# Kernel optimization log

Hardware: AMD Instinct MI355X
Metric: run time of the kernel (lower is better)

Reference implementation:

```python
import jax, jax.numpy as jnp
import numpy as np

B = 1024
NIF = 2048   # n_image_features
V = 10000    # vocab_size
E = 512      # embedding_dim
H = 1024     # hidden_size
L = 32       # max_sentence_length
ND = 3       # num distractors


def _lstm_cell(x, h, c, Wih, Whh, bih, bhh):
    # torch LSTMCell: gates ordered i, f, g, o
    g = x @ Wih.T + bih + h @ Whh.T + bhh
    i, f, gc, o = jnp.split(g, 4, axis=-1)
    c = jax.nn.sigmoid(f) * c + jax.nn.sigmoid(i) * jnp.tanh(gc)
    h = jax.nn.sigmoid(o) * jnp.tanh(c)
    return h, c


def setup_inputs() -> dict:
    key = jax.random.key(0)
    ks = jax.random.split(key, 20)
    s = 0.02
    inp = {
        "target": jax.random.normal(ks[0], (B, NIF), jnp.float32),
        "distractors": jax.random.normal(ks[1], (ND, B, NIF), jnp.float32),
        "start_token_idx": 1,
        "max_sentence_length": L,
        # Sender params
        "W_aff": s * jax.random.normal(ks[2], (H, NIF), jnp.float32),
        "b_aff": jnp.zeros((H,), jnp.float32),
        "emb_s": s * jax.random.normal(ks[3], (V, E), jnp.float32),
        "Wih_s": s * jax.random.normal(ks[4], (4 * H, E), jnp.float32),
        "Whh_s": s * jax.random.normal(ks[5], (4 * H, H), jnp.float32),
        "bih_s": jnp.zeros((4 * H,), jnp.float32),
        "bhh_s": jnp.zeros((4 * H,), jnp.float32),
        "Wp": s * jax.random.normal(ks[6], (V, H), jnp.float32),
        "bp": jnp.zeros((V,), jnp.float32),
        # Receiver params
        "emb_r": s * jax.random.normal(ks[7], (V, E), jnp.float32),
        "Wih_r": s * jax.random.normal(ks[8], (4 * H, E), jnp.float32),
        "Whh_r": s * jax.random.normal(ks[9], (4 * H, H), jnp.float32),
        "bih_r": jnp.zeros((4 * H,), jnp.float32),
        "bhh_r": jnp.zeros((4 * H,), jnp.float32),
        "W_out": s * jax.random.normal(ks[10], (NIF, H), jnp.float32),
        "b_out": jnp.zeros((NIF,), jnp.float32),
    }
    return inp


def reference(target, distractors, start_token_idx, max_sentence_length,
              W_aff, b_aff, emb_s, Wih_s, Whh_s, bih_s, bhh_s, Wp, bp,
              emb_r, Wih_r, Whh_r, bih_r, bhh_r, W_out, b_out):
    Bt = target.shape[0]

    # ---- Sender: greedy decode (eval-mode argmax, matching greedy=True) ----
    h0 = target @ W_aff.T + b_aff
    c0 = jnp.zeros_like(h0)
    w0 = emb_s[jnp.full((Bt,), start_token_idx, dtype=jnp.int32)]

    def send_step(carry, _):
        h, c, w = carry
        h, c = _lstm_cell(w, h, c, Wih_s, Whh_s, bih_s, bhh_s)
        logits = h @ Wp.T + bp                         # [B, V]
        idx = jnp.argmax(logits, axis=-1)              # greedy token
        logp = jnp.take_along_axis(jax.nn.log_softmax(logits, axis=-1),
                                   idx[:, None], axis=-1)[:, 0]
        w = emb_s[idx]
        return (h, c, w), (idx, logp)

    _, (message, logps) = jax.lax.scan(send_step, (h0, c0, w0), None,
                                       length=max_sentence_length)
    message = message.T            # [B, L]
    log_prob = logps[-1]           # log_prob of last sampled word, [B]

    # ---- Receiver: encode message ----
    hr = jnp.zeros((Bt, H), jnp.float32)
    cr = jnp.zeros((Bt, H), jnp.float32)

    def recv_step(carry, w_idx):
        h, c = carry
        h, c = _lstm_cell(emb_r[w_idx], h, c, Wih_r, Whh_r, bih_r, bhh_r)
        return (h, c), None

    (hr, cr), _ = jax.lax.scan(recv_step, (hr, cr), message.T)
    r = hr @ W_out.T + b_out       # [B, NIF]

    # ---- Hinge loss over distractors ----
    r_T = r.T                                       # [NIF, B]
    t_r = target @ r_T                              # [B, B]
    d_r = jnp.einsum('nbf,fc->nbc', distractors, r_T)  # [ND, B, B]
    loss = jnp.sum(jnp.maximum(0.0, 1.0 - t_r[None] + d_r), axis=0)  # [B, B]
    loss = -loss * log_prob        # broadcast [B] over last dim, as in torch
    return jnp.mean(loss)
```

## Files before the change

kernel.cpp:

```cpp
#include <hip/hip_runtime.h>
#include <hip/hip_bf16.h>
#include <cstdint>
#include <cstddef>

#define Bc   1024
#define NIFc 2048
#define Vc   10000
#define Ec   512
#define Hc   1024
#define Lc   32
#define NDc  3
#define G4c  4096
#define NTv  79
#define TMLD 80
#define XLD  3584
#define XOFF 512
#define RLD  1536

typedef __attribute__((ext_vector_type(4))) float f32x4;
typedef __attribute__((ext_vector_type(8))) short s16x8;
typedef __attribute__((ext_vector_type(4))) short s16x4;

__device__ __host__ __forceinline__ int rperm_orig(int p) {
    return ((p >> 4) & 3) * Hc + (p >> 6) * 16 + (p & 15);
}

#define GBM 128
#define GBN 128
#define GBK 64

struct __align__(16) GemmSmem {
    __hip_bfloat16 As[GBM * GBK];
    __hip_bfloat16 Ws[GBN * GBK];
    float smax[GBM];
};

__device__ __forceinline__ void gld_lds16(void* lds, const void* g) {
    __builtin_amdgcn_global_load_lds(
        (const __attribute__((address_space(1))) unsigned int*)g,
        (__attribute__((address_space(3))) unsigned int*)lds,
        16, 0, 0);
}

template<int OBF>
__device__ __forceinline__ void gemm_body(
    GemmSmem& sm,
    const __hip_bfloat16* __restrict__ A, int lda,
    const __hip_bfloat16* __restrict__ W, int ldw,
    const float* __restrict__ bias, void* __restrict__ Cv,
    int M, int N, int K, int bx, int by,
    float* __restrict__ tile_max, int tmld)
{
    __hip_bfloat16* As = sm.As;
    __hip_bfloat16* Ws = sm.Ws;
    float* smax = sm.smax;

    const int tid  = threadIdx.x;
    const int lane = tid & 63;
    const int wave = tid >> 6;
    const int m0 = by * GBM;
    const int n0 = bx * GBN;

    const __hip_bfloat16* ag[4];
    const __hip_bfloat16* wg[4];
    #pragma unroll
    for (int r = 0; r < 4; ++r) {
        int p = r * 256 + tid;
        int m = p >> 3;
        int q = (p & 7) ^ (m & 7);
        int am = m0 + m; if (am >= M) am = M - 1;
        ag[r] = A + (size_t)am * lda + q * 8;
        int wn = n0 + m; if (wn >= N) wn = N - 1;
        wg[r] = W + (size_t)wn * ldw + q * 8;
    }

    f32x4 acc[4][4];
    #pragma unroll
    for (int i = 0; i < 4; ++i)
        #pragma unroll
        for (int j = 0; j < 4; ++j)
            acc[i][j] = (f32x4)(0.0f);

    const int hm = (wave & 1) << 6;
    const int hn = (wave >> 1) << 6;
    const int lm = lane & 15;
    const int quad = lane >> 4;

    const int nk = K >> 6;
    for (int kt = 0; kt < nk; ++kt) {
        __syncthreads();
        #pragma unroll
        for (int r = 0; r < 4; ++r) {
            int ldsbase = (r * 256 + wave * 64) * 8;
            gld_lds16(As + ldsbase, ag[r]);
            gld_lds16(Ws + ldsbase, wg[r]);
            ag[r] += GBK;
            wg[r] += GBK;
        }
        __syncthreads();
        #pragma unroll
        for (int c = 0; c < 2; ++c) {
            s16x8 af[4], wf[4];
            int q = c * 4 + quad;
            #pragma unroll
            for (int i = 0; i < 4; ++i) {
                int m = hm + i * 16 + lm;
                af[i] = *(const s16x8*)(As + ((m << 3) + (q ^ (m & 7))) * 8);
                int n = hn + i * 16 + lm;
                wf[i] = *(const s16x8*)(Ws + ((n << 3) + (q ^ (n & 7))) * 8);
            }
            #pragma unroll
            for (int i = 0; i < 4; ++i)
                #pragma unroll
                for (int j = 0; j < 4; ++j)
                    acc[i][j] = __builtin_amdgcn_mfma_f32_16x16x32_bf16(
                        af[i], wf[j], acc[i][j], 0, 0, 0);
        }
    }

    float rowmax[4][4];
    #pragma unroll
    for (int i = 0; i < 4; ++i)
        #pragma unroll
        for (int rr = 0; rr < 4; ++rr)
            rowmax[i][rr] = -__builtin_inff();

    #pragma unroll
    for (int i = 0; i < 4; ++i) {
        int mbase = m0 + hm + i * 16 + quad * 4;
        #pragma unroll
        for (int j = 0; j < 4; ++j) {
            int n = n0 + hn + j * 16 + lm;
            if (n < N) {
                float bv = bias ? bias[n] : 0.0f;
                #pragma unroll
                for (int rr = 0; rr < 4; ++rr) {
                    float v = acc[i][j][rr] + bv;
                    float vs = v;
                    if (OBF) {
                        __hip_bfloat16 vb = __float2bfloat16(v);
                        vs = __bfloat162float(vb);
                        if (mbase + rr < M)
                            ((__hip_bfloat16*)Cv)[(size_t)(mbase + rr) * N + n] = vb;
                    } else {
                        if (mbase + rr < M)
                            ((float*)Cv)[(size_t)(mbase + rr) * N + n] = v;
                    }
                    rowmax[i][rr] = fmaxf(rowmax[i][rr], vs);
                }
            }
        }
    }

    if (tile_max) {
        #pragma unroll
        for (int i = 0; i < 4; ++i)
            #pragma unroll
            for (int rr = 0; rr < 4; ++rr) {
                float v = rowmax[i][rr];
                v = fmaxf(v, __shfl_xor(v, 1));
                v = fmaxf(v, __shfl_xor(v, 2));
                v = fmaxf(v, __shfl_xor(v, 4));
                v = fmaxf(v, __shfl_xor(v, 8));
                rowmax[i][rr] = v;
            }
        __syncthreads();
        if (hn == 0 && lm == 0) {
            #pragma unroll
            for (int i = 0; i < 4; ++i)
                #pragma unroll
                for (int rr = 0; rr < 4; ++rr)
                    smax[hm + i * 16 + quad * 4 + rr] = rowmax[i][rr];
        }
        __syncthreads();
        if (hn == 64 && lm == 0) {
            #pragma unroll
            for (int i = 0; i < 4; ++i)
                #pragma unroll
                for (int rr = 0; rr < 4; ++rr) {
                    int r = hm + i * 16 + quad * 4 + rr;
                    smax[r] = fmaxf(smax[r], rowmax[i][rr]);
                }
        }
        __syncthreads();
        if (tid < GBM)
            tile_max[(size_t)(m0 + tid) * tmld + bx] = smax[tid];
    }
}

__device__ __forceinline__ void recv_gemm_cell_body(
    GemmSmem& sm,
    const __hip_bfloat16* __restrict__ A,
    const __hip_bfloat16* __restrict__ W,
    const float* __restrict__ biasp,
    const __hip_bfloat16* __restrict__ Xg,
    const int* __restrict__ tok,
    float* __restrict__ cr,
    __hip_bfloat16* __restrict__ xh_out,
    int bx, int by)
{
    __hip_bfloat16* As = sm.As;
    __hip_bfloat16* Ws = sm.Ws;

    const int tid  = threadIdx.x;
    const int lane = tid & 63;
    const int wave = tid >> 6;
    const int m0 = by * GBM;
    const int n0 = bx * GBN;

    const __hip_bfloat16* ag[4];
    const __hip_bfloat16* wg[4];
    #pragma unroll
    for (int r = 0; r < 4; ++r) {
        int p = r * 256 + tid;
        int m = p >> 3;
        int q = (p & 7) ^ (m & 7);
        ag[r] = A + (size_t)(m0 + m) * RLD + q * 8;
        wg[r] = W + (size_t)(n0 + m) * RLD + q * 8;
    }

    f32x4 acc[4][4];
    #pragma unroll
    for (int i = 0; i < 4; ++i)
        #pragma unroll
        for (int j = 0; j < 4; ++j)
            acc[i][j] = (f32x4)(0.0f);

    const int hm = (wave & 1) << 6;
    const int hn = (wave >> 1) << 6;
    const int lm = lane & 15;
    const int quad = lane >> 4;

    for (int kt = 0; kt < Hc / GBK; ++kt) {
        __syncthreads();
        #pragma unroll
        for (int r = 0; r < 4; ++r) {
            int ldsbase = (r * 256 + wave * 64) * 8;
            gld_lds16(As + ldsbase, ag[r]);
            gld_lds16(Ws + ldsbase, wg[r]);
            ag[r] += GBK;
            wg[r] += GBK;
        }
        __syncthreads();
        #pragma unroll
        for (int c = 0; c < 2; ++c) {
            s16x8 af[4], wf[4];
            int q = c * 4 + quad;
            #pragma unroll
            for (int i = 0; i < 4; ++i) {
                int m = hm + i * 16 + lm;
                af[i] = *(const s16x8*)(As + ((m << 3) + (q ^ (m & 7))) * 8);
                int n = hn + i * 16 + lm;
                wf[i] = *(const s16x8*)(Ws + ((n << 3) + (q ^ (n & 7))) * 8);
            }
            #pragma unroll
            for (int i = 0; i < 4; ++i)
                #pragma unroll
                for (int j = 0; j < 4; ++j)
                    acc[i][j] = __builtin_amdgcn_mfma_f32_16x16x32_bf16(
                        af[i], wf[j], acc[i][j], 0, 0, 0);
        }
    }

    const int u = ((n0 + hn) >> 6) * 16 + lm;
    int pc[4];
    float bv[4];
    #pragma unroll
    for (int g = 0; g < 4; ++g) {
        pc[g] = n0 + hn + g * 16 + lm;
        bv[g] = biasp[pc[g]];
    }
    #pragma unroll
    for (int i = 0; i < 4; ++i) {
        #pragma unroll
        for (int rr = 0; rr < 4; ++rr) {
            int b = m0 + hm + i * 16 + quad * 4 + rr;
            const __hip_bfloat16* xr = Xg + (size_t)tok[b] * G4c;
            float gi = acc[i][0][rr] + bv[0] + __bfloat162float(xr[pc[0]]);
            float gf = acc[i][1][rr] + bv[1] + __bfloat162float(xr[pc[1]]);
            float gg = acc[i][2][rr] + bv[2] + __bfloat162float(xr[pc[2]]);
            float go = acc[i][3][rr] + bv[3] + __bfloat162float(xr[pc[3]]);
            float si = 1.0f / (1.0f + expf(-gi));
            float sf = 1.0f / (1.0f + expf(-gf));
            float so = 1.0f / (1.0f + expf(-go));
            size_t cix = (size_t)b * Hc + u;
            float cc = sf * cr[cix] + si * tanhf(gg);
            cr[cix] = cc;
            xh_out[(size_t)b * RLD + Ec + u] = __float2bfloat16(so * tanhf(cc));
        }
    }
}

__global__ __launch_bounds__(256) void gemm_recv_final(
    const __hip_bfloat16* __restrict__ A, const __hip_bfloat16* __restrict__ W,
    const float* __restrict__ biasp, const __hip_bfloat16* __restrict__ Xg,
    const int* __restrict__ tok, float* __restrict__ cr,
    __hip_bfloat16* __restrict__ xh_out)
{
    __shared__ GemmSmem sm;
    recv_gemm_cell_body(sm, A, W, biasp, Xg, tok, cr, xh_out,
                        blockIdx.x & 31, blockIdx.x >> 5);
}

__global__ __launch_bounds__(256) void gemm_bf16_tn(
    const __hip_bfloat16* __restrict__ A, int lda,
    const __hip_bfloat16* __restrict__ W, int ldw,
    const float* __restrict__ bias, float* __restrict__ C,
    int M, int N, int K, float* __restrict__ tile_max, int tmld)
{
    __shared__ GemmSmem sm;
    gemm_body<0>(sm, A, lda, W, ldw, bias, C, M, N, K, blockIdx.x, blockIdx.y,
                 tile_max, tmld);
}

__global__ __launch_bounds__(256) void gemm_bf16_sk2(
    const __hip_bfloat16* __restrict__ A, int lda,
    const __hip_bfloat16* __restrict__ W, int ldw,
    float* __restrict__ Cpart, int M, int N, int Ksub)
{
    __shared__ GemmSmem sm;
    int z = blockIdx.z;
    gemm_body<0>(sm, A + (size_t)z * Ksub, lda, W + (size_t)z * Ksub, ldw,
                 nullptr, Cpart + (size_t)z * M * N, M, N, Ksub, blockIdx.x,
                 blockIdx.y, nullptr, 0);
}

__global__ __launch_bounds__(256) void gemm_tab_h0(
    int nbS, int nbR,
    const __hip_bfloat16* __restrict__ embS, const __hip_bfloat16* __restrict__ embR,
    const __hip_bfloat16* __restrict__ W3x, const __hip_bfloat16* __restrict__ Wr,
    __hip_bfloat16* __restrict__ XgS, __hip_bfloat16* __restrict__ XgR,
    const __hip_bfloat16* __restrict__ target3,
    const __hip_bfloat16* __restrict__ W_aff3, float* __restrict__ gates_p)
{
    __shared__ GemmSmem sm;
    int bid = blockIdx.x;
    if (bid < nbS) {
        gemm_body<1>(sm, embS, Ec, W3x, XLD, nullptr, XgS,
                     Vc, G4c, Ec, bid & 31, bid >> 5, nullptr, 0);
    } else if (bid < nbS + nbR) {
        int rem = bid - nbS;
        gemm_body<1>(sm, embR, Ec, Wr, RLD, nullptr, XgR,
                     Vc, G4c, Ec, rem & 31, rem >> 5, nullptr, 0);
    } else {
        int r2 = bid - nbS - nbR;
        int z = r2 >> 6, rem = r2 & 63;
        gemm_body<0>(sm, target3 + (size_t)z * 3072, 6144,
                     W_aff3 + (size_t)z * 3072, 6144, nullptr,
                     gates_p + (size_t)z * Bc * Hc,
                     Bc, Hc, 3072, rem & 7, rem >> 3, nullptr, 0);
    }
}

template<int LOGBF>
__global__ __launch_bounds__(256) void gemm_fused_step(
    int nb_g,
    const __hip_bfloat16* __restrict__ Ag, const __hip_bfloat16* __restrict__ Wg,
    float* __restrict__ Cg,
    const __hip_bfloat16* __restrict__ Al, const __hip_bfloat16* __restrict__ Wl,
    const float* __restrict__ bl, void* __restrict__ Cl,
    float* __restrict__ tmax)
{
    __shared__ GemmSmem sm;
    int bid = blockIdx.x;
    if (bid < nb_g) {
        gemm_body<0>(sm, Ag, XLD, Wg, XLD, nullptr, Cg,
                     Bc, G4c, 3072, bid & 31, bid >> 5, nullptr, 0);
    } else {
        int rem = bid - nb_g;
        int by = rem / NTv, bx = rem - by * NTv;
        gemm_body<LOGBF>(sm, Al, XLD, Wl, Hc, bl, Cl, Bc, Vc, Hc, bx, by,
                         tmax, TMLD);
    }
}

#define PC0  2097152
#define PC1  6291456
#define PC2  16531456
#define PC3  18628608
#define PC4  20725760
#define PC5  22822912
#define PC6  27017216
#define PC7  29114368
#define PC8  29118464
#define PC9  29122560
#define PC10 34242560
#define PC11 39362560
#define PC12 41459712
#define PC13 47751168

__global__ __launch_bounds__(256) void prep_all_kernel(
    const float* __restrict__ Wih_s, const float* __restrict__ Whh_s,
    const float* __restrict__ Wp, const float* __restrict__ target,
    const float* __restrict__ W_aff, const float* __restrict__ Wih_r,
    const float* __restrict__ Whh_r, const float* __restrict__ W_out,
    const float* __restrict__ bih_s, const float* __restrict__ bhh_s,
    const float* __restrict__ bih_r, const float* __restrict__ bhh_r,
    const float* __restrict__ emb_s, const float* __restrict__ emb_r,
    const float* __restrict__ distr,
    __hip_bfloat16* __restrict__ W3x, __hip_bfloat16* __restrict__ Wp_b,
    __hip_bfloat16* __restrict__ target3, __hip_bfloat16* __restrict__ W_aff3,
    __hip_bfloat16* __restrict__ WihWhh_r, __hip_bfloat16* __restrict__ W_out_b,
    float* __restrict__ bias_s, float* __restrict__ bias_r,
    __hip_bfloat16* __restrict__ embS, __hip_bfloat16* __restrict__ embR,
    __hip_bfloat16* __restrict__ A4b)
{
    int i = blockIdx.x * 256 + threadIdx.x;
    if (i < PC0) {
        W3x[(size_t)(i / Ec) * XLD + (i % Ec)] = __float2bfloat16(Wih_s[i]);
    } else if (i < PC1) {
        int k = i - PC0; int m = k / Hc, c = k - m * Hc;
        float v = Whh_s[k];
        __hip_bfloat16 hi = __float2bfloat16(v);
        float lo = v - __bfloat162float(hi);
        __hip_bfloat16* row = W3x + (size_t)m * XLD + XOFF;
        row[c] = hi; row[Hc + c] = hi; row[2 * Hc + c] = __float2bfloat16(lo);
    } else if (i < PC2) {
        int k = i - PC1;
        Wp_b[k] = __float2bfloat16(Wp[k]);
    } else if (i < PC3) {
        int k = i - PC2; int m = k / NIFc, c = k - m * NIFc;
        float v = target[k];
        __hip_bfloat16 hi = __float2bfloat16(v);
        float lo = v - __bfloat162float(hi);
        __hip_bfloat16* row = target3 + (size_t)m * 6144;
        row[c] = hi; row[NIFc + c] = __float2bfloat16(lo); row[2 * NIFc + c] = hi;
    } else if (i < PC4) {
        int k = i - PC3; int m = k / NIFc, c = k - m * NIFc;
        float v = W_aff[k];
        __hip_bfloat16 hi = __float2bfloat16(v);
        float lo = v - __bfloat162float(hi);
        __hip_bfloat16* row = W_aff3 + (size_t)m * 6144;
        row[c] = hi; row[NIFc + c] = hi; row[2 * NIFc + c] = __float2bfloat16(lo);
    } else if (i < PC5) {
        int k = i - PC4; int p = k / Ec, c = k - p * Ec;
        WihWhh_r[(size_t)p * RLD + c] =
            __float2bfloat16(Wih_r[(size_t)rperm_orig(p) * Ec + c]);
    } else if (i < PC6) {
        int k = i - PC5; int p = k / Hc, c = k - p * Hc;
        WihWhh_r[(size_t)p * RLD + Ec + c] =
            __float2bfloat16(Whh_r[(size_t)rperm_orig(p) * Hc + c]);
    } else if (i < PC7) {
        int k = i - PC6;
        W_out_b[k] = __float2bfloat16(W_out[k]);
    } else if (i < PC8) {
        int k = i - PC7;
        bias_s[k] = bih_s[k] + bhh_s[k];
    } else if (i < PC9) {
        int k = i - PC8; int s = rperm_orig(k);
        bias_r[k] = bih_r[s] + bhh_r[s];
    } else if (i < PC10) {
        int k = i - PC9;
        embS[k] = __float2bfloat16(emb_s[k]);
    } else if (i < PC11) {
        int k = i - PC10;
        embR[k] = __float2bfloat16(emb_r[k]);
    } else if (i < PC12) {
        int k = i - PC11;
        A4b[k] = __float2bfloat16(target[k]);
    } else if (i < PC13) {
        int k = i - PC12;
        A4b[(size_t)Bc * NIFc + k] = __float2bfloat16(distr[k]);
    }
}

__global__ __launch_bounds__(256) void cast2d_kernel(
    const float* __restrict__ in, int ldin,
    __hip_bfloat16* __restrict__ out, int ldo, int coff, int M, int K)
{
    int i = blockIdx.x * 256 + threadIdx.x;
    if (i >= M * K) return;
    int m = i / K, k = i - m * K;
    out[(size_t)m * ldo + coff + k] = __float2bfloat16(in[(size_t)m * ldin + k]);
}

__global__ __launch_bounds__(256) void gather_cast_kernel(
    const float* __restrict__ emb, int E, const int* __restrict__ idx,
    int stride, __hip_bfloat16* __restrict__ out, int ldo, int coff, int Brows)
{
    int i = blockIdx.x * 256 + threadIdx.x;
    if (i >= Brows * E) return;
    int b = i / E, k = i - b * E;
    out[(size_t)b * ldo + coff + k] =
        __float2bfloat16(emb[(size_t)idx[(size_t)b * stride] * E + k]);
}

__device__ __forceinline__ short bf16bits(float x) {
    __hip_bfloat16 t = __float2bfloat16(x);
    return *reinterpret_cast<short*>(&t);
}

__device__ __forceinline__ float b16f(short s) {
    return __bfloat162float(*reinterpret_cast<__hip_bfloat16*>(&s));
}

__global__ __launch_bounds__(256) void lstm_fused_s(
    const float* __restrict__ gp0, const float* __restrict__ gp1,
    const float* __restrict__ bias, float* __restrict__ h,
    float* __restrict__ c, __hip_bfloat16* __restrict__ h3x,
    const __hip_bfloat16* __restrict__ xg, const int* __restrict__ tok,
    int tstride)
{
    int i = blockIdx.x * 256 + threadIdx.x;
    if (i >= Bc * Hc / 4) return;
    int b = i >> 8;
    int j = (i & 255) * 4;
    size_t g0 = (size_t)b * G4c + j;
    f32x4 gi = *(const f32x4*)(gp0 + g0) + *(const f32x4*)(gp1 + g0)
             + *(const f32x4*)(bias + j);
    f32x4 gf = *(const f32x4*)(gp0 + g0 + Hc) + *(const f32x4*)(gp1 + g0 + Hc)
             + *(const f32x4*)(bias + Hc + j);
    f32x4 gg = *(const f32x4*)(gp0 + g0 + 2 * Hc) + *(const f32x4*)(gp1 + g0 + 2 * Hc)
             + *(const f32x4*)(bias + 2 * Hc + j);
    f32x4 go = *(const f32x4*)(gp0 + g0 + 3 * Hc) + *(const f32x4*)(gp1 + g0 + 3 * Hc)
             + *(const f32x4*)(bias + 3 * Hc + j);
    if (xg) {
        const __hip_bfloat16* xr = xg + (size_t)tok[(size_t)b * tstride] * G4c;
        s16x4 xi = *(const s16x4*)(xr + j);
        s16x4 xf = *(const s16x4*)(xr + Hc + j);
        s16x4 xc = *(const s16x4*)(xr + 2 * Hc + j);
        s16x4 xo = *(const s16x4*)(xr + 3 * Hc + j);
        #pragma unroll
        for (int k = 0; k < 4; ++k) {
            gi[k] += b16f(xi[k]);
            gf[k] += b16f(xf[k]);
            gg[k] += b16f(xc[k]);
            go[k] += b16f(xo[k]);
        }
    }
    size_t hix = (size_t)b * Hc + j;
    f32x4 cv = *(const f32x4*)(c + hix);
    f32x4 cn, hv;
    s16x4 hi4, lo4;
    #pragma unroll
    for (int k = 0; k < 4; ++k) {
        float si = 1.0f / (1.0f + expf(-gi[k]));
        float sf = 1.0f / (1.0f + expf(-gf[k]));
        float so = 1.0f / (1.0f + expf(-go[k]));
        float cc = sf * cv[k] + si * tanhf(gg[k]);
        cn[k] = cc;
        float hh = so * tanhf(cc);
        hv[k] = hh;
        hi4[k] = bf16bits(hh);
        lo4[k] = bf16bits(hh - __bfloat162float(__float2bfloat16(hh)));
    }
    *(f32x4*)(c + hix) = cn;
    *(f32x4*)(h + hix) = hv;
    __hip_bfloat16* row = h3x + (size_t)b * XLD + XOFF;
    *(s16x4*)(row + j) = hi4;
    *(s16x4*)(row + Hc + j) = lo4;
    *(s16x4*)(row + 2 * Hc + j) = hi4;
}

__global__ __launch_bounds__(256) void combine_h0_kernel(
    const float* __restrict__ p0, const float* __restrict__ p1,
    const float* __restrict__ bias, float* __restrict__ h,
    __hip_bfloat16* __restrict__ h3x)
{
    int i = blockIdx.x * 256 + threadIdx.x;
    if (i >= Bc * Hc / 4) return;
    int b = i >> 8;
    int j = (i & 255) * 4;
    size_t ix = (size_t)b * Hc + j;
    f32x4 v = *(const f32x4*)(p0 + ix) + *(const f32x4*)(p1 + ix)
            + *(const f32x4*)(bias + j);
    *(f32x4*)(h + ix) = v;
    s16x4 hi4, lo4;
    #pragma unroll
    for (int k = 0; k < 4; ++k) {
        hi4[k] = bf16bits(v[k]);
        lo4[k] = bf16bits(v[k] - __bfloat162float(__float2bfloat16(v[k])));
    }
    __hip_bfloat16* row = h3x + (size_t)b * XLD + XOFF;
    *(s16x4*)(row + j) = hi4;
    *(s16x4*)(row + Hc + j) = lo4;
    *(s16x4*)(row + 2 * Hc + j) = hi4;
}

__global__ __launch_bounds__(256) void lstm_fused_r(
    const float* __restrict__ gp0, const float* __restrict__ gp1,
    const float* __restrict__ bias, float* __restrict__ h,
    float* __restrict__ c, __hip_bfloat16* __restrict__ xh_r,
    const __hip_bfloat16* __restrict__ xg, const int* __restrict__ tok,
    int has_g, const float* __restrict__ emb, const int* __restrict__ msg_next)
{
    int i = blockIdx.x * 256 + threadIdx.x;
    if (i >= Bc * Hc / 4) return;
    int b = i >> 8;
    int j = (i & 255) * 4;
    int pb = (j >> 4) * 64 + (j & 15);
    f32x4 gi = *(const f32x4*)(bias + pb);
    f32x4 gf = *(const f32x4*)(bias + pb + 16);
    f32x4 gg = *(const f32x4*)(bias + pb + 32);
    f32x4 go = *(const f32x4*)(bias + pb + 48);
    if (has_g) {
        size_t g0 = (size_t)b * G4c + pb;
        gi += *(const f32x4*)(gp0 + g0) + *(const f32x4*)(gp1 + g0);
        gf += *(const f32x4*)(gp0 + g0 + 16) + *(const f32x4*)(gp1 + g0 + 16);
        gg += *(const f32x4*)(gp0 + g0 + 32) + *(const f32x4*)(gp1 + g0 + 32);
        go += *(const f32x4*)(gp0 + g0 + 48) + *(const f32x4*)(gp1 + g0 + 48);
    }
    if (xg) {
        const __hip_bfloat16* xr = xg + (size_t)tok[b] * G4c;
        s16x4 xi = *(const s16x4*)(xr + pb);
        s16x4 xf = *(const s16x4*)(xr + pb + 16);
        s16x4 xc = *(const s16x4*)(xr + pb + 32);
        s16x4 xo = *(const s16x4*)(xr + pb + 48);
        #pragma unroll
        for (int k = 0; k < 4; ++k) {
            gi[k] += b16f(xi[k]);
            gf[k] += b16f(xf[k]);
            gg[k] += b16f(xc[k]);
            go[k] += b16f(xo[k]);
        }
    }
    size_t hix = (size_t)b * Hc + j;
    f32x4 cv = *(const f32x4*)(c + hix);
    f32x4 cn, hv;
    s16x4 hb4;
    #pragma unroll
    for (int k = 0; k < 4; ++k) {
        float si = 1.0f / (1.0f + expf(-gi[k]));
        float sf = 1.0f / (1.0f + expf(-gf[k]));
        float so = 1.0f / (1.0f + expf(-go[k]));
        float cc = sf * cv[k] + si * tanhf(gg[k]);
        cn[k] = cc;
        float hh = so * tanhf(cc);
        hv[k] = hh;
        hb4[k] = bf16bits(hh);
    }
    *(f32x4*)(c + hix) = cn;
    *(f32x4*)(h + hix) = hv;
    *(s16x4*)(xh_r + (size_t)b * RLD + Ec + j) = hb4;
    if (!xg && msg_next && j < Ec) {
        int t2 = msg_next[b];
        f32x4 e = *(const f32x4*)(emb + (size_t)t2 * Ec + j);
        s16x4 eb;
        #pragma unroll
        for (int k = 0; k < 4; ++k) eb[k] = bf16bits(e[k]);
        *(s16x4*)(xh_r + (size_t)b * RLD + j) = eb;
    }
}

__global__ __launch_bounds__(256) void argmax_rescore_v3(
    const float* __restrict__ logits, const float* __restrict__ tmax,
    const float* __restrict__ h, const float* __restrict__ Wp,
    const float* __restrict__ bp, const float* __restrict__ emb,
    int* __restrict__ msg_t, float* __restrict__ logp,
    __hip_bfloat16* __restrict__ xdst, int want_logp)
{
    const int b = blockIdx.x;
    const int tid = threadIdx.x;
    const int lane = tid & 63;
    const int wave = tid >> 6;
    const float* row = logits + (size_t)b * Vc;

    __shared__ float stm[128];
    __shared__ float redm[256];
    __shared__ float reds[256];
    __shared__ int   qt[32];
    __shared__ int   nq, cnt;
    __shared__ int   cand[64];
    __shared__ float score[64];
    __shared__ float sbestv;
    __shared__ int   sbestj;

    float tv = (tid < NTv) ? tmax[(size_t)b * TMLD + tid] : -__builtin_inff();
    if (tid < 128) stm[tid] = tv;
    redm[tid] = tv;
    reds[tid] = (tid < NTv) ? tv : 0.0f;
    if (tid == 0) { nq = 0; cnt = 0; }
    __syncthreads();
    #pragma unroll
    for (int s = 128; s > 0; s >>= 1) {
        if (tid < s) {
            redm[tid] = fmaxf(redm[tid], redm[tid + s]);
            reds[tid] += reds[tid + s];
        }
        __syncthreads();
    }
    const float m = redm[0];
    const float spread = m - reds[0] * (1.0f / NTv);
    const float delta = 0.08f * spread + 1e-6f * (1.0f + fabsf(m));

    if (tid < NTv && stm[tid] >= m - delta) {
        int k = atomicAdd(&nq, 1);
        if (k < 32) qt[k] = tid;
    }
    __syncthreads();
    int nqt = nq < 32 ? nq : 32;

    for (int qi = 0; qi < nqt; qi += 2) {
        int ti = qi + (tid >> 7);
        if (ti < nqt) {
            int j = qt[ti] * 128 + (tid & 127);
            if (j < Vc) {
                float v = row[j];
                if (v >= m - delta) {
                    int k = atomicAdd(&cnt, 1);
                    if (k < 64) cand[k] = j;
                }
            }
        }
    }
    __syncthreads();
    int nc = cnt < 64 ? cnt : 64;

    const float* hrow = h + (size_t)b * Hc;
    for (int cix = wave; cix < nc; cix += 4) {
        int j = cand[cix];
        const float* wrow = Wp + (size_t)j * Hc;
        float part = 0.0f;
        #pragma unroll
        for (int kk = 0; kk < 4; ++kk) {
            int k = kk * 256 + lane * 4;
            f32x4 hv = *(const f32x4*)(hrow + k);
            f32x4 wv = *(const f32x4*)(wrow + k);
            part = fmaf(hv.x, wv.x, part);
            part = fmaf(hv.y, wv.y, part);
            part = fmaf(hv.z, wv.z, part);
            part = fmaf(hv.w, wv.w, part);
        }
        #pragma unroll
        for (int off = 1; off < 64; off <<= 1)
            part += __shfl_xor(part, off);
        if (lane == 0) score[cix] = part + bp[j];
    }
    __syncthreads();
    if (tid == 0) {
        float bv = -__builtin_inff();
        int bj = 0x7fffffff;
        for (int cix = 0; cix < nc; ++cix) {
            float v = score[cix];
            int j = cand[cix];
            if (v > bv || (v == bv && j < bj)) { bv = v; bj = j; }
        }
        sbestv = bv;
        sbestj = bj;
        msg_t[b] = bj;
    }
    __syncthreads();
    const int bestj = sbestj;

    if (want_logp) {
        float s = 0.0f;
        const f32x4* row4 = (const f32x4*)row;
        for (int j = tid; j < Vc / 4; j += 256) {
            f32x4 v = row4[j];
            s += expf(v.x - m) + expf(v.y - m) + expf(v.z - m) + expf(v.w - m);
        }
        redm[tid] = s;
        __syncthreads();
        #pragma unroll
        for (int st = 128; st > 0; st >>= 1) {
            if (tid < st) redm[tid] += redm[tid + st];
            __syncthreads();
        }
        if (tid == 0) logp[b] = sbestv - (m + logf(redm[0]));
    }

    if (xdst && tid < 128) {
        int k = tid * 4;
        f32x4 e = *(const f32x4*)(emb + (size_t)bestj * Ec + k);
        s16x4 h4;
        #pragma unroll
        for (int kk = 0; kk < 4; ++kk) h4[kk] = bf16bits(e[kk]);
        *(s16x4*)(xdst + (size_t)b * XLD + k) = h4;
    }
}

template<int LGBF>
__global__ __launch_bounds__(256) void argmax_cell_recv(
    int nb_r,
    const __hip_bfloat16* __restrict__ Ar, const __hip_bfloat16* __restrict__ Wr,
    const float* __restrict__ biasrp, const __hip_bfloat16* __restrict__ Xgr,
    const int* __restrict__ tokr, float* __restrict__ cr,
    __hip_bfloat16* __restrict__ xh_out,
    const void* __restrict__ logits_v, const float* __restrict__ tmax,
    const float* __restrict__ h, const float* __restrict__ Wp,
    const float* __restrict__ bp, int* __restrict__ msg_t,
    float* __restrict__ logp, int want_logp,
    int do_s, const float* __restrict__ gp0,
    const float* __restrict__ bias_s, float* __restrict__ h_s,
    float* __restrict__ c_s, __hip_bfloat16* __restrict__ h3x,
    const __hip_bfloat16* __restrict__ Xg_s)
{
    __shared__ GemmSmem sm;
    __shared__ int nq, cnt, sbestj;
    __shared__ float sbestv;

    if ((int)blockIdx.x < nb_r) {
        recv_gemm_cell_body(sm, Ar, Wr, biasrp, Xgr, tokr, cr, xh_out,
                            blockIdx.x & 31, blockIdx.x >> 5);
        return;
    }
    const int b = blockIdx.x - nb_r;
    const int tid = threadIdx.x;
    const int lane = tid & 63;
    const int wave = tid >> 6;
    const __hip_bfloat16* rowb = (const __hip_bfloat16*)logits_v + (size_t)b * Vc;
    const float* rowf = (const float*)logits_v + (size_t)b * Vc;

    float* stm  = (float*)sm.As;
    float* redm = stm + 128;
    float* reds = redm + 256;
    int*   qt   = (int*)(reds + 256);
    int*   cand = qt + 32;
    float* score= (float*)(cand + 64);

    float tv = (tid < NTv) ? tmax[(size_t)b * TMLD + tid] : -__builtin_inff();
    if (tid < 128) stm[tid] = tv;
    redm[tid] = tv;
    reds[tid] = (tid < NTv) ? tv : 0.0f;
    if (tid == 0) { nq = 0; cnt = 0; }
    __syncthreads();
    #pragma unroll
    for (int s = 128; s > 0; s >>= 1) {
        if (tid < s) {
            redm[tid] = fmaxf(redm[tid], redm[tid + s]);
            reds[tid] += reds[tid + s];
        }
        __syncthreads();
    }
    const float m = redm[0];
    const float spread = m - reds[0] * (1.0f / NTv);
    const float delta = 0.08f * spread + 1e-6f * (1.0f + fabsf(m));

    if (tid < NTv && stm[tid] >= m - delta) {
        int k = atomicAdd(&nq, 1);
        if (k < 32) qt[k] = tid;
    }
    __syncthreads();
    int nqt = nq < 32 ? nq : 32;

    for (int qi = 0; qi < nqt; qi += 2) {
        int ti = qi + (tid >> 7);
        if (ti < nqt) {
            int j = qt[ti] * 128 + (tid & 127);
            if (j < Vc) {
                float v = LGBF ? __bfloat162float(rowb[j]) : rowf[j];
                if (v >= m - delta) {
                    int k = atomicAdd(&cnt, 1);
                    if (k < 64) cand[k] = j;
                }
            }
        }
    }
    __syncthreads();
    int nc = cnt < 64 ? cnt : 64;

    const float* hrow = h + (size_t)b * Hc;
    for (int cix = wave; cix < nc; cix += 4) {
        int j = cand[cix];
        const float* wrow = Wp + (size_t)j * Hc;
        float part = 0.0f;
        #pragma unroll
        for (int kk = 0; kk < 4; ++kk) {
            int k = kk * 256 + lane * 4;
            f32x4 hv = *(const f32x4*)(hrow + k);
            f32x4 wv = *(const f32x4*)(wrow + k);
            part = fmaf(hv.x, wv.x, part);
            part = fmaf(hv.y, wv.y, part);
            part = fmaf(hv.z, wv.z, part);
            part = fmaf(hv.w, wv.w, part);
        }
        #pragma unroll
        for (int off = 1; off < 64; off <<= 1)
            part += __shfl_xor(part, off);
        if (lane == 0) score[cix] = part + bp[j];
    }
    __syncthreads();
    if (tid == 0) {
        float bv = -__builtin_inff();
        int bj = 0x7fffffff;
        for (int cix = 0; cix < nc; ++cix) {
            float v = score[cix];
            int j = cand[cix];
            if (v > bv || (v == bv && j < bj)) { bv = v; bj = j; }
        }
        sbestv = bv;
        sbestj = bj;
        msg_t[b] = bj;
    }
    __syncthreads();
    const int tok = sbestj;

    if (!LGBF && want_logp) {
        float s = 0.0f;
        const f32x4* row4 = (const f32x4*)rowf;
        for (int j = tid; j < Vc / 4; j += 256) {
            f32x4 v = row4[j];
            s += expf(v.x - m) + expf(v.y - m) + expf(v.z - m) + expf(v.w - m);
        }
        redm[tid] = s;
        __syncthreads();
        #pragma unroll
        for (int st = 128; st > 0; st >>= 1) {
            if (tid < st) redm[tid] += redm[tid + st];
            __syncthreads();
        }
        if (tid == 0) logp[b] = sbestv - (m + logf(redm[0]));
        __syncthreads();
    }

    if (do_s) {
        const int j = tid * 4;
        size_t g0 = (size_t)b * G4c + j;
        f32x4 gi = *(const f32x4*)(gp0 + g0) + *(const f32x4*)(bias_s + j);
        f32x4 gf = *(const f32x4*)(gp0 + g0 + Hc) + *(const f32x4*)(bias_s + Hc + j);
        f32x4 gg = *(const f32x4*)(gp0 + g0 + 2 * Hc) + *(const f32x4*)(bias_s + 2 * Hc + j);
        f32x4 go = *(const f32x4*)(gp0 + g0 + 3 * Hc) + *(const f32x4*)(bias_s + 3 * Hc + j);
        const __hip_bfloat16* xr = Xg_s + (size_t)tok * G4c;
        s16x4 xi = *(const s16x4*)(xr + j);
        s16x4 xf = *(const s16x4*)(xr + Hc + j);
        s16x4 xc = *(const s16x4*)(xr + 2 * Hc + j);
        s16x4 xo = *(const s16x4*)(xr + 3 * Hc + j);
        size_t hix = (size_t)b * Hc + j;
        f32x4 cv = *(const f32x4*)(c_s + hix);
        f32x4 cn, hv;
        s16x4 hi4, lo4;
        #pragma unroll
        for (int k = 0; k < 4; ++k) {
            float gik = gi[k] + b16f(xi[k]);
            float gfk = gf[k] + b16f(xf[k]);
            float ggk = gg[k] + b16f(xc[k]);
            float gok = go[k] + b16f(xo[k]);
            float si = 1.0f / (1.0f + expf(-gik));
            float sf = 1.0f / (1.0f + expf(-gfk));
            float so = 1.0f / (1.0f + expf(-gok));
            float cc = sf * cv[k] + si * tanhf(ggk);
            cn[k] = cc;
            float hh = so * tanhf(cc);
            hv[k] = hh;
            hi4[k] = bf16bits(hh);
            lo4[k] = bf16bits(hh - __bfloat162float(__float2bfloat16(hh)));
        }
        *(f32x4*)(c_s + hix) = cn;
        *(f32x4*)(h_s + hix) = hv;
        __hip_bfloat16* orow = h3x + (size_t)b * XLD + XOFF;
        *(s16x4*)(orow + j) = hi4;
        *(s16x4*)(orow + Hc + j) = lo4;
        *(s16x4*)(orow + 2 * Hc + j) = hi4;
    }
}

__global__ __launch_bounds__(256) void hinge_kernel(
    const float* __restrict__ S, const float* __restrict__ logp,
    float* __restrict__ partials, int Bn)
{
    int tid = threadIdx.x;
    int n = Bn * Bn;
    float acc = 0.0f;
    for (int idx = blockIdx.x * 256 + tid; idx < n; idx += gridDim.x * 256) {
        int j = idx & (Bn - 1);
        float s0 = S[idx];
        float l = fmaxf(0.0f, 1.0f - s0 + S[n + idx])
                + fmaxf(0.0f, 1.0f - s0 + S[2 * n + idx])
                + fmaxf(0.0f, 1.0f - s0 + S[3 * n + idx]);
        acc += l * logp[j];
    }
    __shared__ float sv[256];
    sv[tid] = acc;
    __syncthreads();
    for (int s = 128; s > 0; s >>= 1) {
        if (tid < s) sv[tid] += sv[tid + s];
        __syncthreads();
    }
    if (tid == 0) partials[blockIdx.x] = sv[0];
}

__global__ __launch_bounds__(256) void final_reduce_kernel(
    const float* __restrict__ partials, int np, float* __restrict__ out,
    float scale)
{
    int tid = threadIdx.x;
    float acc = 0.0f;
    for (int i = tid; i < np; i += 256) acc += partials[i];
    __shared__ float sv[256];
    sv[tid] = acc;
    __syncthreads();
    for (int s = 128; s > 0; s >>= 1) {
        if (tid < s) sv[tid] += sv[tid + s];
        __syncthreads();
    }
    if (tid == 0) out[0] = sv[0] * scale;
}

extern "C" void kernel_launch(void* const* d_in, const int* in_sizes, int n_in,
                              void* d_out, int out_size, void* d_ws, size_t ws_size,
                              hipStream_t stream)
{
    (void)in_sizes; (void)n_in; (void)out_size;

    const float* target  = (const float*)d_in[0];
    const float* distr   = (const float*)d_in[1];
    const int*   start_t = (const int*)d_in[2];
    const float* W_aff = (const float*)d_in[4];
    const float* b_aff = (const float*)d_in[5];
    const float* emb_s = (const float*)d_in[6];
    const float* Wih_s = (const float*)d_in[7];
    const float* Whh_s = (const float*)d_in[8];
    const float* bih_s = (const float*)d_in[9];
    const float* bhh_s = (const float*)d_in[10];
    const float* Wp    = (const float*)d_in[11];
    const float* bp    = (const float*)d_in[12];
    const float* emb_r = (const float*)d_in[13];
    const float* Wih_r = (const float*)d_in[14];
    const float* Whh_r = (const float*)d_in[15];
    const float* bih_r = (const float*)d_in[16];
    const float* bhh_r = (const float*)d_in[17];
    const float* W_out = (const float*)d_in[18];
    const float* b_out = (const float*)d_in[19];

    dim3 blk(256);

    char* b0 = (char*)d_ws;
    size_t off = 0;
    auto take = [&](size_t bytes) -> char* {
        char* p = b0 + off;
        off += (bytes + 511) & ~(size_t)511;
        return p;
    };
    const size_t MB = 1024 * 1024;
    __hip_bfloat16* W3x     = (__hip_bfloat16*)take((size_t)G4c * XLD * 2);
    __hip_bfloat16* Wp_b    = (__hip_bfloat16*)take((size_t)Vc * Hc * 2);
    __hip_bfloat16* WihWhh_r= (__hip_bfloat16*)take((size_t)G4c * RLD * 2);
    __hip_bfloat16* W_out_b = (__hip_bfloat16*)take((size_t)NIFc * Hc * 2);
    __hip_bfloat16* h3x     = (__hip_bfloat16*)take((size_t)Bc * XLD * 2);
    __hip_bfloat16* xh_rA   = (__hip_bfloat16*)take((size_t)Bc * RLD * 2);
    __hip_bfloat16* xh_rB   = (__hip_bfloat16*)take((size_t)Bc * RLD * 2);
    float* gates_p = (float*)take((size_t)2 * Bc * G4c * 4);
    float* h_s    = (float*)take((size_t)Bc * Hc * 4);
    float* c_s    = (float*)take((size_t)Bc * Hc * 4);
    float* hr     = (float*)take((size_t)Bc * Hc * 4);
    float* cr     = (float*)take((size_t)Bc * Hc * 4);
    float* logp   = (float*)take(Bc * 4);
    int*   msg    = (int*)take((size_t)Lc * Bc * 4);
    float* parts  = (float*)take(1024 * 4);
    float* bias_s = (float*)take(G4c * 4);
    float* bias_r = (float*)take(G4c * 4);
    float* tilemax= (float*)take((size_t)Bc * TMLD * 4);
    char*  U      = take(48 * MB);

    __hip_bfloat16* Xg_s = (__hip_bfloat16*)take((size_t)Vc * G4c * 2);
    const int use_tab_s = (off <= ws_size);
    __hip_bfloat16* Xg_r = (__hip_bfloat16*)take((size_t)Vc * G4c * 2);
    const int use_tab_r = (off <= ws_size);
    const int use_merged = use_tab_s && use_tab_r;
    __hip_bfloat16* A4b_ws = (__hip_bfloat16*)take((size_t)4 * Bc * NIFc * 2);
    __hip_bfloat16* r_b_ws = (__hip_bfloat16*)take((size_t)Bc * NIFc * 2);
    const int use_extra = (off <= ws_size);

    __hip_bfloat16* target3 = (__hip_bfloat16*)U;
    __hip_bfloat16* W_aff3  = (__hip_bfloat16*)(U + 13 * MB);
    __hip_bfloat16* emb_bS  = (__hip_bfloat16*)(U + 26 * MB);
    __hip_bfloat16* emb_bR  = (__hip_bfloat16*)(U + 36 * MB);
    float*          logits  = (float*)U;
    __hip_bfloat16* A4b_u   = (__hip_bfloat16*)U;
    float*          r_f     = (float*)(U + 17 * MB);
    __hip_bfloat16* r_b_u   = (__hip_bfloat16*)(U + 26 * MB);
    float*          S       = (float*)(U + 31 * MB);

    __hip_bfloat16* A4b = use_extra ? A4b_ws : A4b_u;
    __hip_bfloat16* r_b = use_extra ? r_b_ws : r_b_u;

    const int base_blocks  = (PC11 + 255) / 256;
    const int extra_blocks = (PC13 + 255) / 256;
    prep_all_kernel<<<use_extra ? extra_blocks : base_blocks, blk, 0, stream>>>(
        Wih_s, Whh_s, Wp, target, W_aff, Wih_r, Whh_r, W_out,
        bih_s, bhh_s, bih_r, bhh_r, emb_s, emb_r, distr,
        W3x, Wp_b, target3, W_aff3, WihWhh_r, W_out_b, bias_s, bias_r,
        emb_bS, emb_bR, A4b);

    const int nbS = use_tab_s ? 2528 : 0;
    const int nbR = use_tab_r ? 2528 : 0;
    gemm_tab_h0<<<nbS + nbR + 128, blk, 0, stream>>>(
        nbS, nbR, emb_bS, emb_bR, W3x, WihWhh_r, Xg_s, Xg_r,
        target3, W_aff3, gates_p);

    combine_h0_kernel<<<(Bc * Hc / 4 + 255) / 256, blk, 0, stream>>>(
        gates_p, gates_p + (size_t)Bc * Hc, b_aff, h_s, h3x);
    hipMemsetAsync(c_s, 0, (size_t)Bc * Hc * 4, stream);

    if (use_merged) {
        hipMemsetAsync(cr, 0, (size_t)Bc * Hc * 4, stream);
        hipMemsetAsync(xh_rA, 0, (size_t)Bc * RLD * 2, stream);

        gemm_bf16_sk2<<<dim3(G4c / GBN, Bc / GBM, 2), blk, 0, stream>>>(
            h3x + XOFF, XLD, W3x + XOFF, XLD, gates_p, Bc, G4c, 1536);
        lstm_fused_s<<<(Bc * Hc / 4 + 255) / 256, blk, 0, stream>>>(
            gates_p, gates_p + (size_t)Bc * G4c, bias_s, h_s, c_s, h3x,
            Xg_s, start_t, 0);

        for (int t = 0; t < Lc; ++t) {
            const int do_g = (t < Lc - 1);
            const int nb_r = (t >= 1) ? 256 : 0;
            const int k = t - 1;
            const __hip_bfloat16* rin = (k & 1) ? xh_rB : xh_rA;
            __hip_bfloat16* rout = (k & 1) ? xh_rA : xh_rB;
            if (t < Lc - 1) {
                gemm_fused_step<1><<<do_g * 256 + 632, blk, 0, stream>>>(
                    do_g ? 256 : 0,
                    h3x + XOFF, W3x + XOFF, gates_p,
                    h3x + XOFF, Wp_b, bp, (void*)logits, tilemax);
                argmax_cell_recv<1><<<nb_r + Bc, blk, 0, stream>>>(
                    nb_r, rin + Ec, WihWhh_r + Ec, bias_r, Xg_r,
                    (t >= 1) ? msg + (t - 1) * Bc : msg, cr, rout,
                    (const void*)logits, tilemax, h_s, Wp, bp, msg + t * Bc,
                    logp, 0, 1, gates_p, bias_s, h_s, c_s, h3x, Xg_s);
            } else {
                gemm_fused_step<0><<<632, blk, 0, stream>>>(
                    0,
                    h3x + XOFF, W3x + XOFF, gates_p,
                    h3x + XOFF, Wp_b, bp, (void*)logits, tilemax);
                argmax_cell_recv<0><<<nb_r + Bc, blk, 0, stream>>>(
                    nb_r, rin + Ec, WihWhh_r + Ec, bias_r, Xg_r,
                    msg + (t - 1) * Bc, cr, rout,
                    (const void*)logits, tilemax, h_s, Wp, bp, msg + t * Bc,
                    logp, 1, 0, gates_p, bias_s, h_s, c_s, h3x, Xg_s);
            }
        }
        gemm_recv_final<<<256, blk, 0, stream>>>(
            xh_rB + Ec, WihWhh_r + Ec, bias_r, Xg_r, msg + (Lc - 1) * Bc,
            cr, xh_rA);
    } else {
        if (!use_tab_s)
            gather_cast_kernel<<<(Bc * Ec + 255) / 256, blk, 0, stream>>>(
                emb_s, Ec, start_t, 0, h3x, XLD, 0, Bc);

        for (int t = 0; t < Lc; ++t) {
            if (use_tab_s) {
                gemm_bf16_sk2<<<dim3(G4c / GBN, Bc / GBM, 2), blk, 0, stream>>>(
                    h3x + XOFF, XLD, W3x + XOFF, XLD, gates_p, Bc, G4c, 1536);
                lstm_fused_s<<<(Bc * Hc / 4 + 255) / 256, blk, 0, stream>>>(
                    gates_p, gates_p + (size_t)Bc * G4c, bias_s, h_s, c_s, h3x,
                    Xg_s, (t == 0) ? start_t : (msg + (t - 1) * Bc),
                    (t == 0) ? 0 : 1);
            } else {
                gemm_bf16_sk2<<<dim3(G4c / GBN, Bc / GBM, 2), blk, 0, stream>>>(
                    h3x, XLD, W3x, XLD, gates_p, Bc, G4c, 1792);
                lstm_fused_s<<<(Bc * Hc / 4 + 255) / 256, blk, 0, stream>>>(
                    gates_p, gates_p + (size_t)Bc * G4c, bias_s, h_s, c_s, h3x,
                    nullptr, nullptr, 0);
            }
            gemm_bf16_tn<<<dim3((Vc + GBN - 1) / GBN, Bc / GBM), blk, 0, stream>>>(
                h3x + XOFF, XLD, Wp_b, Hc, bp, logits, Bc, Vc, Hc, tilemax, TMLD);
            argmax_rescore_v3<<<Bc, blk, 0, stream>>>(
                logits, tilemax, h_s, Wp, bp, emb_s, msg + t * Bc, logp,
                (!use_tab_s && t < Lc - 1) ? h3x : nullptr,
                (t == Lc - 1) ? 1 : 0);
        }

        hipMemsetAsync(hr, 0, (size_t)Bc * Hc * 4, stream);
        hipMemsetAsync(cr, 0, (size_t)Bc * Hc * 4, stream);
        hipMemsetAsync(xh_rA, 0, (size_t)Bc * RLD * 2, stream);
        if (!use_tab_r)
            gather_cast_kernel<<<(Bc * Ec + 255) / 256, blk, 0, stream>>>(
                emb_r, Ec, msg, 1, xh_rA, RLD, 0, Bc);
        for (int t = 0; t < Lc; ++t) {
            if (use_tab_r) {
                if (t > 0)
                    gemm_bf16_sk2<<<dim3(G4c / GBN, Bc / GBM, 2), blk, 0, stream>>>(
                        xh_rA + Ec, RLD, WihWhh_r + Ec, RLD, gates_p, Bc, G4c, 512);
                lstm_fused_r<<<(Bc * Hc / 4 + 255) / 256, blk, 0, stream>>>(
                    gates_p, gates_p + (size_t)Bc * G4c, bias_r, hr, cr, xh_rA,
                    Xg_r, msg + t * Bc, (t > 0) ? 1 : 0, nullptr, nullptr);
            } else {
                gemm_bf16_sk2<<<dim3(G4c / GBN, Bc / GBM, 2), blk, 0, stream>>>(
                    xh_rA, RLD, WihWhh_r, RLD, gates_p, Bc, G4c, 768);
                lstm_fused_r<<<(Bc * Hc / 4 + 255) / 256, blk, 0, stream>>>(
                    gates_p, gates_p + (size_t)Bc * G4c, bias_r, hr, cr, xh_rA,
                    nullptr, nullptr, 1, emb_r,
                    (t < Lc - 1) ? (msg + (t + 1) * Bc) : nullptr);
            }
        }
    }

    gemm_bf16_tn<<<dim3(NIFc / GBN, Bc / GBM), blk, 0, stream>>>(
        xh_rA + Ec, RLD, W_out_b, Hc, b_out, r_f, Bc, NIFc, Hc, nullptr, 0);

    if (!use_extra) {
        cast2d_kernel<<<(Bc * NIFc + 255) / 256, blk, 0, stream>>>(
            target, NIFc, A4b, NIFc, 0, Bc, NIFc);
        cast2d_kernel<<<(NDc * Bc * NIFc + 255) / 256, blk, 0, stream>>>(
            distr, NIFc, A4b + (size_t)Bc * NIFc, NIFc, 0, NDc * Bc, NIFc);
    }
    cast2d_kernel<<<(Bc * NIFc + 255) / 256, blk, 0, stream>>>(
        r_f, NIFc, r_b, NIFc, 0, Bc, NIFc);
    gemm_bf16_tn<<<dim3(Bc / GBN, 4 * Bc / GBM), blk, 0, stream>>>(
        A4b, NIFc, r_b, NIFc, nullptr, S, 4 * Bc, Bc, NIFc, nullptr, 0);

    hinge_kernel<<<1024, blk, 0, stream>>>(S, logp, parts, Bc);
    final_reduce_kernel<<<1, blk, 0, stream>>>(
        parts, 1024, (float*)d_out, -1.0f / ((float)Bc * (float)Bc));
}
```

Baseline: 4.486 ms.

## Move receiver LSTM step into fused GEMM launch and emit bf16 output directly

```diff
diff --git a/kernel.cpp b/kernel.cpp
--- a/kernel.cpp
+++ b/kernel.cpp
@@ -32,7 +32,6 @@
 struct __align__(16) GemmSmem {
     __hip_bfloat16 As[GBM * GBK];
     __hip_bfloat16 Ws[GBN * GBK];
-    float smax[GBM];
 };
 
 __device__ __forceinline__ void gld_lds16(void* lds, const void* g) {
@@ -53,7 +52,6 @@
 {
     __hip_bfloat16* As = sm.As;
     __hip_bfloat16* Ws = sm.Ws;
-    float* smax = sm.smax;
 
     const int tid  = threadIdx.x;
     const int lane = tid & 63;
@@ -153,6 +151,7 @@
     }
 
     if (tile_max) {
+        float* smax = (float*)sm.As;
         #pragma unroll
         for (int i = 0; i < 4; ++i)
             #pragma unroll
@@ -313,6 +312,17 @@
                  tile_max, tmld);
 }
 
+__global__ __launch_bounds__(256) void gemm_bf16_tn_obf(
+    const __hip_bfloat16* __restrict__ A, int lda,
+    const __hip_bfloat16* __restrict__ W, int ldw,
+    const float* __restrict__ bias, __hip_bfloat16* __restrict__ C,
+    int M, int N, int K)
+{
+    __shared__ GemmSmem sm;
+    gemm_body<1>(sm, A, lda, W, ldw, bias, C, M, N, K, blockIdx.x, blockIdx.y,
+                 nullptr, 0);
+}
+
 __global__ __launch_bounds__(256) void gemm_bf16_sk2(
     const __hip_bfloat16* __restrict__ A, int lda,
     const __hip_bfloat16* __restrict__ W, int ldw,
@@ -359,18 +369,26 @@
     float* __restrict__ Cg,
     const __hip_bfloat16* __restrict__ Al, const __hip_bfloat16* __restrict__ Wl,
     const float* __restrict__ bl, void* __restrict__ Cl,
-    float* __restrict__ tmax)
+    float* __restrict__ tmax,
+    const __hip_bfloat16* __restrict__ Ar, const __hip_bfloat16* __restrict__ Wr,
+    const float* __restrict__ biasrp, const __hip_bfloat16* __restrict__ Xgr,
+    const int* __restrict__ tokr, float* __restrict__ cr,
+    __hip_bfloat16* __restrict__ xh_out)
 {
     __shared__ GemmSmem sm;
     int bid = blockIdx.x;
     if (bid < nb_g) {
         gemm_body<0>(sm, Ag, XLD, Wg, XLD, nullptr, Cg,
                      Bc, G4c, 3072, bid & 31, bid >> 5, nullptr, 0);
-    } else {
+    } else if (bid < nb_g + 632) {
         int rem = bid - nb_g;
         int by = rem / NTv, bx = rem - by * NTv;
         gemm_body<LOGBF>(sm, Al, XLD, Wl, Hc, bl, Cl, Bc, Vc, Hc, bx, by,
                          tmax, TMLD);
+    } else {
+        int rem = bid - nb_g - 632;
+        recv_gemm_cell_body(sm, Ar, Wr, biasrp, Xgr, tokr, cr, xh_out,
+                            rem & 31, rem >> 5);
     }
 }
 
@@ -770,12 +788,7 @@
 }
 
 template<int LGBF>
-__global__ __launch_bounds__(256) void argmax_cell_recv(
-    int nb_r,
-    const __hip_bfloat16* __restrict__ Ar, const __hip_bfloat16* __restrict__ Wr,
-    const float* __restrict__ biasrp, const __hip_bfloat16* __restrict__ Xgr,
-    const int* __restrict__ tokr, float* __restrict__ cr,
-    __hip_bfloat16* __restrict__ xh_out,
+__global__ __launch_bounds__(256) void argmax_cell(
     const void* __restrict__ logits_v, const float* __restrict__ tmax,
     const float* __restrict__ h, const float* __restrict__ Wp,
     const float* __restrict__ bp, int* __restrict__ msg_t,
@@ -785,28 +798,21 @@
     float* __restrict__ c_s, __hip_bfloat16* __restrict__ h3x,
     const __hip_bfloat16* __restrict__ Xg_s)
 {
-    __shared__ GemmSmem sm;
-    __shared__ int nq, cnt, sbestj;
-    __shared__ float sbestv;
-
-    if ((int)blockIdx.x < nb_r) {
-        recv_gemm_cell_body(sm, Ar, Wr, biasrp, Xgr, tokr, cr, xh_out,
-                            blockIdx.x & 31, blockIdx.x >> 5);
-        return;
-    }
-    const int b = blockIdx.x - nb_r;
+    const int b = blockIdx.x;
     const int tid = threadIdx.x;
     const int lane = tid & 63;
     const int wave = tid >> 6;
     const __hip_bfloat16* rowb = (const __hip_bfloat16*)logits_v + (size_t)b * Vc;
     const float* rowf = (const float*)logits_v + (size_t)b * Vc;
 
-    float* stm  = (float*)sm.As;
-    float* redm = stm + 128;
-    float* reds = redm + 256;
-    int*   qt   = (int*)(reds + 256);
-    int*   cand = qt + 32;
-    float* score= (float*)(cand + 64);
+    __shared__ float stm[128];
+    __shared__ float redm[256];
+    __shared__ float reds[256];
+    __shared__ int   qt[32];
+    __shared__ int   cand[64];
+    __shared__ float score[64];
+    __shared__ int   nq, cnt, sbestj;
+    __shared__ float sbestv;
 
     float tv = (tid < NTv) ? tmax[(size_t)b * TMLD + tid] : -__builtin_inff();
     if (tid < 128) stm[tid] = tv;
@@ -1057,7 +1063,6 @@
     __hip_bfloat16* emb_bR  = (__hip_bfloat16*)(U + 36 * MB);
     float*          logits  = (float*)U;
     __hip_bfloat16* A4b_u   = (__hip_bfloat16*)U;
-    float*          r_f     = (float*)(U + 17 * MB);
     __hip_bfloat16* r_b_u   = (__hip_bfloat16*)(U + 26 * MB);
     float*          S       = (float*)(U + 31 * MB);
 
@@ -1093,29 +1098,28 @@
             Xg_s, start_t, 0);
 
         for (int t = 0; t < Lc; ++t) {
-            const int do_g = (t < Lc - 1);
+            const int nb_g = (t < Lc - 1) ? 256 : 0;
             const int nb_r = (t >= 1) ? 256 : 0;
             const int k = t - 1;
             const __hip_bfloat16* rin = (k & 1) ? xh_rB : xh_rA;
             __hip_bfloat16* rout = (k & 1) ? xh_rA : xh_rB;
+            const int* tokr = (t >= 1) ? (msg + (t - 1) * Bc) : msg;
             if (t < Lc - 1) {
-                gemm_fused_step<1><<<do_g * 256 + 632, blk, 0, stream>>>(
-                    do_g ? 256 : 0,
+                gemm_fused_step<1><<<nb_g + 632 + nb_r, blk, 0, stream>>>(
+                    nb_g,
                     h3x + XOFF, W3x + XOFF, gates_p,
-                    h3x + XOFF, Wp_b, bp, (void*)logits, tilemax);
-                argmax_cell_recv<1><<<nb_r + Bc, blk, 0, stream>>>(
-                    nb_r, rin + Ec, WihWhh_r + Ec, bias_r, Xg_r,
-                    (t >= 1) ? msg + (t - 1) * Bc : msg, cr, rout,
+                    h3x + XOFF, Wp_b, bp, (void*)logits, tilemax,
+                    rin + Ec, WihWhh_r + Ec, bias_r, Xg_r, tokr, cr, rout);
+                argmax_cell<1><<<Bc, blk, 0, stream>>>(
                     (const void*)logits, tilemax, h_s, Wp, bp, msg + t * Bc,
                     logp, 0, 1, gates_p, bias_s, h_s, c_s, h3x, Xg_s);
             } else {
-                gemm_fused_step<0><<<632, blk, 0, stream>>>(
+                gemm_fused_step<0><<<632 + nb_r, blk, 0, stream>>>(
                     0,
                     h3x + XOFF, W3x + XOFF, gates_p,
-                    h3x + XOFF, Wp_b, bp, (void*)logits, tilemax);
-                argmax_cell_recv<0><<<nb_r + Bc, blk, 0, stream>>>(
-                    nb_r, rin + Ec, WihWhh_r + Ec, bias_r, Xg_r,
-                    msg + (t - 1) * Bc, cr, rout,
+                    h3x + XOFF, Wp_b, bp, (void*)logits, tilemax,
+                    rin + Ec, WihWhh_r + Ec, bias_r, Xg_r, tokr, cr, rout);
+                argmax_cell<0><<<Bc, blk, 0, stream>>>(
                     (const void*)logits, tilemax, h_s, Wp, bp, msg + t * Bc,
                     logp, 1, 0, gates_p, bias_s, h_s, c_s, h3x, Xg_s);
             }
@@ -1176,8 +1180,8 @@
         }
     }
 
-    gemm_bf16_tn<<<dim3(NIFc / GBN, Bc / GBM), blk, 0, stream>>>(
-        xh_rA + Ec, RLD, W_out_b, Hc, b_out, r_f, Bc, NIFc, Hc, nullptr, 0);
+    gemm_bf16_tn_obf<<<dim3(NIFc / GBN, Bc / GBM), blk, 0, stream>>>(
+        xh_rA + Ec, RLD, W_out_b, Hc, b_out, r_b, Bc, NIFc, Hc);
 
     if (!use_extra) {
         cast2d_kernel<<<(Bc * NIFc + 255) / 256, blk, 0, stream>>>(
@@ -1185,8 +1189,6 @@
         cast2d_kernel<<<(NDc * Bc * NIFc + 255) / 256, blk, 0, stream>>>(
             distr, NIFc, A4b + (size_t)Bc * NIFc, NIFc, 0, NDc * Bc, NIFc);
     }
-    cast2d_kernel<<<(Bc * NIFc + 255) / 256, blk, 0, stream>>>(
-        r_f, NIFc, r_b, NIFc, 0, Bc, NIFc);
     gemm_bf16_tn<<<dim3(Bc / GBN, 4 * Bc / GBM), blk, 0, stream>>>(
         A4b, NIFc, r_b, NIFc, nullptr, S, 4 * Bc, Bc, NIFc, nullptr, 0);
 
```

Result: no change. 4.480 ms (-0.1%).
